# Kernel optimization log

Measured on AMD Instinct MI355X. Metric: run time of the kernel, lower is better.

## Reference

```python
import jax, jax.numpy as jnp
import numpy as np

LATENT = 2000
N_GROUPS = 10000  # loci_count // window_size
KERNEL = 20       # window_size * 2; per-group input length is 1 so out length == KERNEL
BATCH = 128
EPS = 1e-5
SLOPE = 0.1


def setup_inputs() -> dict:
    key = jax.random.key(0)
    k1, k2, k3, k4, k5 = jax.random.split(key, 5)
    return {
        "z": jax.random.normal(k1, (BATCH, LATENT), dtype=jnp.float32),
        "W_fc": jax.random.normal(k2, (N_GROUPS, LATENT), dtype=jnp.float32) * 0.02,
        "b_fc": jax.random.normal(k3, (N_GROUPS,), dtype=jnp.float32) * 0.02,
        "gamma": jnp.ones((N_GROUPS,), dtype=jnp.float32),
        "beta": jnp.zeros((N_GROUPS,), dtype=jnp.float32),
        "conv_w": jax.random.normal(k4, (N_GROUPS, KERNEL), dtype=jnp.float32) * 0.1,
        "conv_b": jax.random.normal(k5, (N_GROUPS,), dtype=jnp.float32) * 0.02,
    }


def reference(z, W_fc, b_fc, gamma, beta, conv_w, conv_b):
    # Linear: (B, L) @ (L, G) -> (B, G)
    h = jnp.einsum("bl,gl->bg", z, W_fc) + b_fc
    # BatchNorm1d (training mode: biased batch statistics, eps=1e-5)
    mean = jnp.mean(h, axis=0)
    var = jnp.mean(jnp.square(h - mean), axis=0)
    h = (h - mean) * jax.lax.rsqrt(var + EPS) * gamma + beta
    h = jnp.where(h >= 0, h, SLOPE * h)  # LeakyReLU(0.1)
    # Grouped ConvTranspose1d with per-group input length 1 degenerates to
    # an outer product per channel: y[b,g,k] = h[b,g]*w[g,k] + b[g]
    y = h[:, :, None] * conv_w[None, :, :] + conv_b[None, :, None]  # (B, G, K)
    y = jnp.where(y >= 0, y, SLOPE * y)  # LeakyReLU(0.1)
    out = jax.nn.sigmoid(y.reshape(z.shape[0], N_GROUPS * KERNEL))
    return out
```

## Files before the change

### kernel.cpp

```cpp
#include <hip/hip_runtime.h>
#include <hip/hip_bf16.h>
#include <stdint.h>

#define BATCH 128
#define LAT   2000
#define NG    10000
#define KW    20
#define OUTW  (NG * KW)
#define EPSV  1e-5f

#define NKT   32
#define EG    16
#define WPAD  2056
#define HR_STRIDE 132

typedef __bf16 bf16x8 __attribute__((ext_vector_type(8)));
typedef float  f32x4  __attribute__((ext_vector_type(4)));

__device__ __forceinline__ ushort f2bf(float f) {
  uint32_t u = __builtin_bit_cast(uint32_t, f);
  u = (u + 0x7FFFu + ((u >> 16) & 1u)) >> 16;
  return (ushort)u;
}

__device__ __forceinline__ int4 pack8(const float* p) {
  float4 f0 = *(const float4*)p;
  float4 f1 = *(const float4*)(p + 4);
  int4 v;
  v.x = (int)((uint32_t)f2bf(f0.x) | ((uint32_t)f2bf(f0.y) << 16));
  v.y = (int)((uint32_t)f2bf(f0.z) | ((uint32_t)f2bf(f0.w) << 16));
  v.z = (int)((uint32_t)f2bf(f1.x) | ((uint32_t)f2bf(f1.y) << 16));
  v.w = (int)((uint32_t)f2bf(f1.z) | ((uint32_t)f2bf(f1.w) << 16));
  return v;
}

__global__ __launch_bounds__(256) void zprep_kernel(
    const float* __restrict__ zp, int4* __restrict__ zlin) {
  const int cg = blockIdx.x * 256 + threadIdx.x;
  const int r  = cg >> 8;
  const int ck = cg & 255;
  const int k0 = ck * 8;
  int4 v = make_int4(0, 0, 0, 0);
  if (k0 < LAT) v = pack8(zp + (size_t)r * LAT + k0);
  const int kt = ck >> 3, kk = (ck >> 2) & 1, q = ck & 3;
  const int dst = ((kt * 2 + kk) * 8 + (r >> 4)) * 64 + q * 16 + (r & 15);
  zlin[dst] = v;
}

__global__ __launch_bounds__(512, 2) void fused16_kernel(
    const int4* __restrict__ zlin, const float* __restrict__ wp,
    const float* __restrict__ gammap, const float* __restrict__ betap,
    const float* __restrict__ convwp, const float* __restrict__ convbp,
    float* __restrict__ out) {
  const int tid = threadIdx.x;
  const int g0  = blockIdx.x * EG;

  __shared__ __attribute__((aligned(16))) ushort Wl[EG * WPAD];
  __shared__ float  h_raw[EG * HR_STRIDE];
  __shared__ float4 cw_s[EG * 5];
  __shared__ float  cb_s[EG];
  __shared__ float  scale_s[EG];
  __shared__ float  shift_s[EG];

  if (tid < EG * 5)
    cw_s[tid] = *(const float4*)(convwp + (size_t)g0 * KW + tid * 4);
  if (tid < EG) cb_s[tid] = convbp[g0 + tid];

#pragma unroll
  for (int i = 0; i < 8; ++i) {
    int cc  = i * 512 + tid;
    int row = cc >> 8;
    int c   = cc & 255;
    int kt  = c >> 3, j = c & 7;
    int k0  = kt * 64 + j * 8;
    int4 v  = make_int4(0, 0, 0, 0);
    if (k0 < LAT) v = pack8(wp + (size_t)(g0 + row) * LAT + k0);
    *(int4*)&Wl[row * WPAD + kt * 64 + j * 8] = v;
  }

  const int lane = tid & 63;
  const int w    = tid >> 6;
  const int q    = lane >> 4;
  const int cl   = lane & 15;
  const int rb   = w * 16 + cl;

  const int4* zw = zlin + (size_t)w * 64 + lane;
  const ushort* wl = &Wl[cl * WPAD];

  f32x4 acc = {0.f, 0.f, 0.f, 0.f};

  int4 za0 = zw[0],    za1 = zw[512];
  int4 zb0 = zw[1024], zb1 = zw[1536];
  int4 zc0 = zw[2048], zc1 = zw[2560];
  int4 zd0 = zw[3072], zd1 = zw[3584];

  __syncthreads();

#pragma unroll 4
  for (int kt = 0; kt < NKT; ++kt) {
    const int tp = (kt + 4 < NKT) ? (kt + 4) : kt;
    int4 ne0 = zw[(size_t)(tp * 2 + 0) * 512];
    int4 ne1 = zw[(size_t)(tp * 2 + 1) * 512];

    bf16x8 a0 = *(const bf16x8*)&wl[kt * 64 + q * 8];
    bf16x8 a1 = *(const bf16x8*)&wl[kt * 64 + (4 + q) * 8];

    acc = __builtin_amdgcn_mfma_f32_16x16x32_bf16(
        a0, __builtin_bit_cast(bf16x8, za0), acc, 0, 0, 0);
    acc = __builtin_amdgcn_mfma_f32_16x16x32_bf16(
        a1, __builtin_bit_cast(bf16x8, za1), acc, 0, 0, 0);

    za0 = zb0; za1 = zb1;
    zb0 = zc0; zb1 = zc1;
    zc0 = zd0; zc1 = zd1;
    zd0 = ne0; zd1 = ne1;
  }

#pragma unroll
  for (int r = 0; r < 4; ++r)
    h_raw[(q * 4 + r) * HR_STRIDE + rb] = acc[r];
  __syncthreads();

  {
    const int gl = tid >> 5;
    const int bb = (tid & 31) * 4;
    const float4 a = *(const float4*)&h_raw[gl * HR_STRIDE + bb];
    float sm = a.x + a.y + a.z + a.w;
    float sq = a.x * a.x + a.y * a.y + a.z * a.z + a.w * a.w;
#pragma unroll
    for (int m = 1; m < 32; m <<= 1) {
      sm += __shfl_xor(sm, m);
      sq += __shfl_xor(sq, m);
    }
    if ((tid & 31) == 0) {
      float mean = sm * (1.f / 128.f);
      float var  = sq * (1.f / 128.f) - mean * mean;
      var = (var < 0.f) ? 0.f : var;
      float inv   = __builtin_amdgcn_rsqf(var + EPSV);
      float scale = inv * gammap[g0 + gl];
      scale_s[gl] = scale;
      shift_s[gl] = betap[g0 + gl] - mean * scale;
    }
  }
  __syncthreads();

  if (tid < 480) {
    const int col4 = tid % 80;
    const int r0   = tid / 80;
    const int gl   = col4 / 5;
    const float4 w4  = cw_s[col4];
    const float  cb  = cb_s[gl];
    const float  scl = scale_s[gl];
    const float  sft = shift_s[gl];
    const float* hsrc = &h_raw[gl * HR_STRIDE];
    float* obase = out + (size_t)g0 * KW + (size_t)col4 * 4;
    for (int j = 0; j < 22; ++j) {
      const int row = j * 6 + r0;
      if (row < BATCH) {
        float h = hsrc[row];
        h = fmaf(h, scl, sft);
        h = fmaxf(h, h * 0.1f);
        float y0 = fmaf(h, w4.x, cb);
        float y1 = fmaf(h, w4.y, cb);
        float y2 = fmaf(h, w4.z, cb);
        float y3 = fmaf(h, w4.w, cb);
        y0 = fmaxf(y0, y0 * 0.1f);
        y1 = fmaxf(y1, y1 * 0.1f);
        y2 = fmaxf(y2, y2 * 0.1f);
        y3 = fmaxf(y3, y3 * 0.1f);
        float4 ov;
        ov.x = __builtin_amdgcn_rcpf(1.f + exp2f(y0 * -1.44269504f));
        ov.y = __builtin_amdgcn_rcpf(1.f + exp2f(y1 * -1.44269504f));
        ov.z = __builtin_amdgcn_rcpf(1.f + exp2f(y2 * -1.44269504f));
        ov.w = __builtin_amdgcn_rcpf(1.f + exp2f(y3 * -1.44269504f));
        *(float4*)(obase + (size_t)row * OUTW) = ov;
      }
    }
  }
}

#define BKF 64
__global__ __launch_bounds__(256, 2) void fused_decoder_kernel(
    const float* __restrict__ zp, const float* __restrict__ wp,
    const float* __restrict__ gammap, const float* __restrict__ betap,
    const float* __restrict__ convwp, const float* __restrict__ convbp,
    float* __restrict__ out) {
  const int tid = threadIdx.x;
  const int g0  = blockIdx.x * 32;

  __shared__ ushort As[BATCH * BKF];
  __shared__ ushort Bs[32 * BKF];
  __shared__ float statS[2][2][16];
  __shared__ float statQ[2][2][16];

  const int lane = tid & 63;
  const int w    = tid >> 6;
  const int wm   = w & 1;
  const int wn   = w >> 1;
  const int q    = lane >> 4;
  const int cl   = lane & 15;

  f32x4 acc[4];
  const f32x4 vzero = {0.f, 0.f, 0.f, 0.f};
#pragma unroll
  for (int i = 0; i < 4; ++i) acc[i] = vzero;

  for (int it = 0; it < 32; ++it) {
    const int k0 = it * BKF;
    __syncthreads();
#pragma unroll
    for (int i = 0; i < 4; ++i) {
      int c = i * 256 + tid;
      int r = c >> 3, sc = c & 7;
      int gk = k0 + sc * 8;
      int4 v = make_int4(0, 0, 0, 0);
      if (gk < LAT) v = pack8(zp + (size_t)r * LAT + gk);
      *(int4*)&As[r * BKF + ((sc ^ (r & 7)) << 3)] = v;
    }
    {
      int r = tid >> 3, sc = tid & 7;
      int g  = g0 + r;
      int gk = k0 + sc * 8;
      int4 v = make_int4(0, 0, 0, 0);
      if (gk < LAT && g < NG) v = pack8(wp + (size_t)g * LAT + gk);
      *(int4*)&Bs[r * BKF + ((sc ^ (r & 7)) << 3)] = v;
    }
    __syncthreads();
#pragma unroll
    for (int kk = 0; kk < 2; ++kk) {
      int sc = kk * 4 + q;
      bf16x8 af[4], bfr;
#pragma unroll
      for (int mt = 0; mt < 4; ++mt) {
        int ra = wm * 64 + mt * 16 + cl;
        af[mt] = *(const bf16x8*)&As[ra * BKF + ((sc ^ (ra & 7)) << 3)];
      }
      {
        int rbx = wn * 16 + cl;
        bfr = *(const bf16x8*)&Bs[rbx * BKF + ((sc ^ (rbx & 7)) << 3)];
      }
#pragma unroll
      for (int mt = 0; mt < 4; ++mt)
        acc[mt] = __builtin_amdgcn_mfma_f32_16x16x32_bf16(af[mt], bfr,
                                                          acc[mt], 0, 0, 0);
    }
  }

  float s = 0.f, ss = 0.f;
#pragma unroll
  for (int mt = 0; mt < 4; ++mt)
#pragma unroll
    for (int r = 0; r < 4; ++r) {
      float v = acc[mt][r];
      s += v; ss += v * v;
    }
  s += __shfl_xor(s, 16); ss += __shfl_xor(ss, 16);
  s += __shfl_xor(s, 32); ss += __shfl_xor(ss, 32);
  if (q == 0) { statS[wm][wn][cl] = s; statQ[wm][wn][cl] = ss; }
  __syncthreads();

  const int gcol = g0 + wn * 16 + cl;
  const int gc   = (gcol < NG) ? gcol : (NG - 1);
  float S = statS[0][wn][cl] + statS[1][wn][cl];
  float Q = statQ[0][wn][cl] + statQ[1][wn][cl];
  float mean = S * (1.f / 128.f);
  float var  = Q * (1.f / 128.f) - mean * mean;
  var = (var < 0.f) ? 0.f : var;
  float inv = __builtin_amdgcn_rsqf(var + EPSV);
  float ga = gammap[gc], be = betap[gc], cb = convbp[gc];
  float wv[KW];
  {
    const float4* pw = (const float4*)(convwp + (size_t)gc * KW);
#pragma unroll
    for (int j = 0; j < 5; ++j) {
      float4 f = pw[j];
      wv[4 * j] = f.x; wv[4 * j + 1] = f.y;
      wv[4 * j + 2] = f.z; wv[4 * j + 3] = f.w;
    }
  }
  float scale = inv * ga;
  float shift = be - mean * scale;
  const bool ok = (gcol < NG);
#pragma unroll
  for (int mt = 0; mt < 4; ++mt) {
#pragma unroll
    for (int r = 0; r < 4; ++r) {
      float h = acc[mt][r] * scale + shift;
      h = fmaxf(h, h * 0.1f);
      int b = wm * 64 + mt * 16 + q * 4 + r;
      float4 ov[5];
#pragma unroll
      for (int j = 0; j < 5; ++j) {
        float y0 = h * wv[4 * j]     + cb;
        float y1 = h * wv[4 * j + 1] + cb;
        float y2 = h * wv[4 * j + 2] + cb;
        float y3 = h * wv[4 * j + 3] + cb;
        y0 = fmaxf(y0, y0 * 0.1f);
        y1 = fmaxf(y1, y1 * 0.1f);
        y2 = fmaxf(y2, y2 * 0.1f);
        y3 = fmaxf(y3, y3 * 0.1f);
        ov[j].x = __builtin_amdgcn_rcpf(1.f + exp2f(y0 * -1.44269504f));
        ov[j].y = __builtin_amdgcn_rcpf(1.f + exp2f(y1 * -1.44269504f));
        ov[j].z = __builtin_amdgcn_rcpf(1.f + exp2f(y2 * -1.44269504f));
        ov[j].w = __builtin_amdgcn_rcpf(1.f + exp2f(y3 * -1.44269504f));
      }
      if (ok) {
        float4* po = (float4*)(out + (size_t)b * OUTW + (size_t)gcol * KW);
#pragma unroll
        for (int j = 0; j < 5; ++j) po[j] = ov[j];
      }
    }
  }
}

extern "C" void kernel_launch(void* const* d_in, const int* in_sizes, int n_in,
                              void* d_out, int out_size, void* d_ws, size_t ws_size,
                              hipStream_t stream) {
  const float* z     = (const float*)d_in[0];
  const float* W     = (const float*)d_in[1];
  const float* gamma = (const float*)d_in[3];
  const float* beta  = (const float*)d_in[4];
  const float* convw = (const float*)d_in[5];
  const float* convb = (const float*)d_in[6];
  float* out = (float*)d_out;

  const size_t zlin_bytes = (size_t)BATCH * 256 * 16;

  if (ws_size >= zlin_bytes) {
    int4* zlin = (int4*)d_ws;
    zprep_kernel<<<128, 256, 0, stream>>>(z, zlin);
    fused16_kernel<<<NG / EG, 512, 0, stream>>>(zlin, W, gamma, beta,
                                                convw, convb, out);
  } else {
    fused_decoder_kernel<<<(NG + 31) / 32, 256, 0, stream>>>(
        z, W, gamma, beta, convw, convb, out);
  }
}
```

Baseline: 198.7 us.

## Split K reduction across two wave halves with 1024-thread blocks

The fused kernel now runs 1024 threads per block. The 16 waves form two halves that each accumulate half of the K tiles of the bf16 MFMA GEMM, and the partial results are summed through shared memory. The BN statistics reduction now uses one wave per group, and the epilogue spreads output rows over 960 threads. The aim is more waves in flight to hide z global-load latency and speed up the W staging and the output writes. The cost is an extra barrier and shared-memory accumulate, and launch_bounds(1024,4) tightens the per-thread register budget.

Result: no change. 201.6 us (+1.5%).

```diff
diff --git a/kernel.cpp b/kernel.cpp
--- a/kernel.cpp
+++ b/kernel.cpp
@@ -47,7 +47,7 @@
   zlin[dst] = v;
 }
 
-__global__ __launch_bounds__(512, 2) void fused16_kernel(
+__global__ __launch_bounds__(1024, 4) void fused16_kernel(
     const int4* __restrict__ zlin, const float* __restrict__ wp,
     const float* __restrict__ gammap, const float* __restrict__ betap,
     const float* __restrict__ convwp, const float* __restrict__ convbp,
@@ -67,8 +67,8 @@
   if (tid < EG) cb_s[tid] = convbp[g0 + tid];
 
 #pragma unroll
-  for (int i = 0; i < 8; ++i) {
-    int cc  = i * 512 + tid;
+  for (int i = 0; i < 4; ++i) {
+    int cc  = i * 1024 + tid;
     int row = cc >> 8;
     int c   = cc & 255;
     int kt  = c >> 3, j = c & 7;
@@ -80,30 +80,34 @@
 
   const int lane = tid & 63;
   const int w    = tid >> 6;
+  const int wg   = w & 7;
+  const int half = w >> 3;
   const int q    = lane >> 4;
   const int cl   = lane & 15;
-  const int rb   = w * 16 + cl;
-
-  const int4* zw = zlin + (size_t)w * 64 + lane;
+  const int rb   = wg * 16 + cl;
+  const int t0   = half * 16;
+
+  const int4* zw = zlin + (size_t)wg * 64 + lane;
   const ushort* wl = &Wl[cl * WPAD];
 
   f32x4 acc = {0.f, 0.f, 0.f, 0.f};
 
-  int4 za0 = zw[0],    za1 = zw[512];
-  int4 zb0 = zw[1024], zb1 = zw[1536];
-  int4 zc0 = zw[2048], zc1 = zw[2560];
-  int4 zd0 = zw[3072], zd1 = zw[3584];
+  int4 za0 = zw[(t0 * 2 + 0) * 512], za1 = zw[(t0 * 2 + 1) * 512];
+  int4 zb0 = zw[(t0 * 2 + 2) * 512], zb1 = zw[(t0 * 2 + 3) * 512];
+  int4 zc0 = zw[(t0 * 2 + 4) * 512], zc1 = zw[(t0 * 2 + 5) * 512];
+  int4 zd0 = zw[(t0 * 2 + 6) * 512], zd1 = zw[(t0 * 2 + 7) * 512];
 
   __syncthreads();
 
 #pragma unroll 4
-  for (int kt = 0; kt < NKT; ++kt) {
-    const int tp = (kt + 4 < NKT) ? (kt + 4) : kt;
-    int4 ne0 = zw[(size_t)(tp * 2 + 0) * 512];
-    int4 ne1 = zw[(size_t)(tp * 2 + 1) * 512];
-
-    bf16x8 a0 = *(const bf16x8*)&wl[kt * 64 + q * 8];
-    bf16x8 a1 = *(const bf16x8*)&wl[kt * 64 + (4 + q) * 8];
+  for (int i = 0; i < 16; ++i) {
+    const int t  = t0 + i;
+    const int tp = (i + 4 < 16) ? (t + 4) : t;
+    int4 ne0 = zw[(tp * 2 + 0) * 512];
+    int4 ne1 = zw[(tp * 2 + 1) * 512];
+
+    bf16x8 a0 = *(const bf16x8*)&wl[t * 64 + q * 8];
+    bf16x8 a1 = *(const bf16x8*)&wl[t * 64 + (4 + q) * 8];
 
     acc = __builtin_amdgcn_mfma_f32_16x16x32_bf16(
         a0, __builtin_bit_cast(bf16x8, za0), acc, 0, 0, 0);
@@ -116,35 +120,43 @@
     zd0 = ne0; zd1 = ne1;
   }
 
-#pragma unroll
-  for (int r = 0; r < 4; ++r)
-    h_raw[(q * 4 + r) * HR_STRIDE + rb] = acc[r];
+  if (half == 0) {
+#pragma unroll
+    for (int r = 0; r < 4; ++r)
+      h_raw[(q * 4 + r) * HR_STRIDE + rb] = acc[r];
+  }
+  __syncthreads();
+  if (half == 1) {
+#pragma unroll
+    for (int r = 0; r < 4; ++r)
+      h_raw[(q * 4 + r) * HR_STRIDE + rb] += acc[r];
+  }
   __syncthreads();
 
   {
-    const int gl = tid >> 5;
-    const int bb = (tid & 31) * 4;
-    const float4 a = *(const float4*)&h_raw[gl * HR_STRIDE + bb];
-    float sm = a.x + a.y + a.z + a.w;
-    float sq = a.x * a.x + a.y * a.y + a.z * a.z + a.w * a.w;
-#pragma unroll
-    for (int m = 1; m < 32; m <<= 1) {
+    const int gw = w;
+    const int l  = lane;
+    const float2 a = *(const float2*)&h_raw[gw * HR_STRIDE + l * 2];
+    float sm = a.x + a.y;
+    float sq = a.x * a.x + a.y * a.y;
+#pragma unroll
+    for (int m = 1; m < 64; m <<= 1) {
       sm += __shfl_xor(sm, m);
       sq += __shfl_xor(sq, m);
     }
-    if ((tid & 31) == 0) {
+    if (l == 0) {
       float mean = sm * (1.f / 128.f);
       float var  = sq * (1.f / 128.f) - mean * mean;
       var = (var < 0.f) ? 0.f : var;
       float inv   = __builtin_amdgcn_rsqf(var + EPSV);
-      float scale = inv * gammap[g0 + gl];
-      scale_s[gl] = scale;
-      shift_s[gl] = betap[g0 + gl] - mean * scale;
-    }
-  }
-  __syncthreads();
-
-  if (tid < 480) {
+      float scale = inv * gammap[g0 + gw];
+      scale_s[gw] = scale;
+      shift_s[gw] = betap[g0 + gw] - mean * scale;
+    }
+  }
+  __syncthreads();
+
+  if (tid < 960) {
     const int col4 = tid % 80;
     const int r0   = tid / 80;
     const int gl   = col4 / 5;
@@ -154,8 +166,8 @@
     const float  sft = shift_s[gl];
     const float* hsrc = &h_raw[gl * HR_STRIDE];
     float* obase = out + (size_t)g0 * KW + (size_t)col4 * 4;
-    for (int j = 0; j < 22; ++j) {
-      const int row = j * 6 + r0;
+    for (int j = 0; j < 11; ++j) {
+      const int row = j * 12 + r0;
       if (row < BATCH) {
         float h = hsrc[row];
         h = fmaf(h, scl, sft);
@@ -329,8 +341,8 @@
   if (ws_size >= zlin_bytes) {
     int4* zlin = (int4*)d_ws;
     zprep_kernel<<<128, 256, 0, stream>>>(z, zlin);
-    fused16_kernel<<<NG / EG, 512, 0, stream>>>(zlin, W, gamma, beta,
-                                                convw, convb, out);
+    fused16_kernel<<<NG / EG, 1024, 0, stream>>>(zlin, W, gamma, beta,
+                                                 convw, convb, out);
   } else {
     fused_decoder_kernel<<<(NG + 31) / 32, 256, 0, stream>>>(
         z, W, gamma, beta, convw, convb, out);
```
